# Kernel optimization log

Hardware: AMD Instinct MI355X
Metric: run time of the kernel (lower is better)

Reference implementation:

```python
import jax, jax.numpy as jnp
import numpy as np
import math

LMAX = 2            # input lmax
LMAX_OUT = 2 * LMAX # gaunt product output lmax
RES_BETA = 20
RES_ALPHA = 39
N = 2048
MUL = 64
C = 64
BRANCHES = [(1, 1), (1, -1), (-1, 1)]  # (p_val1, p_val2) per branch


def _real_sh_grid(lmax, res_beta, res_alpha):
    """Real orthonormal spherical harmonics on a Gauss-Legendre x uniform-alpha grid.
    Returns Y [(lmax+1)^2, res_beta, res_alpha] and quadrature weights qw [res_beta]
    (beta GL weight times 2*pi/res_alpha alpha weight)."""
    x, w = np.polynomial.legendre.leggauss(res_beta)  # x = cos(beta)
    phi = np.linspace(0.0, 2.0 * np.pi, res_alpha, endpoint=False)
    # associated Legendre P[l, m] on x via standard recurrences
    P = np.zeros((lmax + 1, lmax + 1, res_beta))
    P[0, 0] = 1.0
    s = np.sqrt(1.0 - x ** 2)
    for m in range(1, lmax + 1):
        P[m, m] = -(2 * m - 1) * s * P[m - 1, m - 1]
    for m in range(lmax):
        P[m + 1, m] = (2 * m + 1) * x * P[m, m]
    for m in range(lmax + 1):
        for l in range(m + 2, lmax + 1):
            P[l, m] = ((2 * l - 1) * x * P[l - 1, m] - (l + m - 1) * P[l - 2, m]) / (l - m)
    Y = np.zeros(((lmax + 1) ** 2, res_beta, res_alpha))
    idx = 0
    for l in range(lmax + 1):
        for m in range(-l, l + 1):
            am = abs(m)
            K = math.sqrt((2 * l + 1) / (4 * math.pi) * math.factorial(l - am) / math.factorial(l + am))
            if m == 0:
                ang = np.ones(res_alpha)
            elif m > 0:
                ang = math.sqrt(2.0) * np.cos(m * phi)
            else:
                ang = math.sqrt(2.0) * np.sin(am * phi)
            Y[idx] = K * P[l, am][:, None] * ang[None, :]
            idx += 1
    qw = w * (2.0 * np.pi / res_alpha)
    return Y.astype(np.float32), qw.astype(np.float32)


def setup_inputs() -> dict:
    key = jax.random.key(0)
    k1, k2, k3, k4, k5 = jax.random.split(key, 5)
    # inputs carry both parities per l: [N, mul, parity(2), (lmax+1)^2]
    x1 = jax.random.normal(k1, (N, MUL, 2, (LMAX + 1) ** 2), dtype=jnp.float32)
    x2 = jax.random.normal(k2, (N, MUL, 2, (LMAX + 1) ** 2), dtype=jnp.float32)
    # per-branch, per-l linear weights (e3nn Linear mixes multiplicities within each irrep)
    W1 = jax.random.normal(k3, (3, LMAX + 1, MUL, C), dtype=jnp.float32)
    W2 = jax.random.normal(k4, (3, LMAX + 1, MUL, C), dtype=jnp.float32)
    Wout = jax.random.normal(k5, (3, LMAX_OUT + 1, C, C), dtype=jnp.float32)
    Yfull, qw = _real_sh_grid(LMAX_OUT, RES_BETA, RES_ALPHA)
    Y_in = jnp.asarray(Yfull[: (LMAX + 1) ** 2])   # [9, B, A]
    Y_out = jnp.asarray(Yfull)                     # [25, B, A]
    return {"x1": x1, "x2": x2, "W1": W1, "W2": W2, "Wout": Wout,
            "Y_in": Y_in, "Y_out": Y_out, "qw": jnp.asarray(qw)}


def _project(x, W, p_val):
    """e3nn Linear to s2_irreps(LMAX, p_val)*C: for each l, take the input block with
    parity p_val*(-1)^l and mix multiplicities. x [N,mul,2,L2], W [L, mul, C] -> [N, C, L2]."""
    blocks = []
    inv_sqrt_mul = 1.0 / np.sqrt(x.shape[1])
    for l in range(LMAX + 1):
        pidx = 0 if p_val * ((-1) ** l) == 1 else 1  # 0 = even, 1 = odd parity slot
        sl = slice(l * l, (l + 1) * (l + 1))
        blocks.append(jnp.einsum('nmk,mc->nck', x[:, :, pidx, sl], W[l]) * inv_sqrt_mul)
    return jnp.concatenate(blocks, axis=-1)  # [N, C, (LMAX+1)^2]


def _gaunt_branch(x1, x2, W1b, W2b, Woutb, p1, p2, Y_in, Y_out, qw):
    c1 = _project(x1, W1b, p1)                      # [N, C, 9]
    c2 = _project(x2, W2b, p2)
    # SH -> grid (inverse spherical transform)
    s1 = jnp.einsum('ncl,lba->ncba', c1, Y_in)      # [N, C, B, A]
    s2 = jnp.einsum('ncl,lba->ncba', c2, Y_in)
    # pointwise multiply on S2, then grid -> SH (forward transform w/ quadrature)
    co = jnp.einsum('ncba,lba,b->ncl', s1 * s2, Y_out, qw)  # [N, C, 25]
    # linear_out: per-l [C -> C] mixing
    inv_sqrt_c = 1.0 / np.sqrt(co.shape[1])
    outs = []
    for l in range(LMAX_OUT + 1):
        sl = slice(l * l, (l + 1) * (l + 1))
        outs.append(jnp.einsum('nck,cd->ndk', co[:, :, sl], Woutb[l]) * inv_sqrt_c)
    return jnp.concatenate(outs, axis=-1)           # [N, C, 25]


def reference(x1, x2, W1, W2, Wout, Y_in, Y_out, qw):
    outs = [_gaunt_branch(x1, x2, W1[b], W2[b], Wout[b], p1, p2, Y_in, Y_out, qw)
            for b, (p1, p2) in enumerate(BRANCHES)]
    return jnp.stack(outs, axis=1)                  # [N, 3, C, 25] (concat over parities)
```

## Files before the change

kernel.cpp:

```cpp
#include <hip/hip_runtime.h>
#include <utility>


#define NN 2048

__host__ __device__ constexpr int l_of9(int i)  { return i < 1 ? 0 : (i < 4 ? 1 : 2); }
__host__ __device__ constexpr int l_of25(int k) { return k < 1 ? 0 : (k < 4 ? 1 : (k < 9 ? 2 : (k < 16 ? 3 : 4))); }
__host__ __device__ constexpr int iabs_(int v)  { return v < 0 ? -v : v; }

__host__ __device__ constexpr bool gmask(int k, int i, int j) {
    const int l3 = l_of25(k), m3 = k - l3 * l3 - l3;
    const int l1 = l_of9(i),  m1 = i - l1 * l1 - l1;
    const int l2 = l_of9(j),  m2 = j - l2 * l2 - l2;
    if (((l1 + l2 + l3) & 1) != 0) return false;
    if (l3 > l1 + l2 || l3 < iabs_(l1 - l2)) return false;
    const int am3 = iabs_(m3);
    return (am3 == iabs_(m1 + m2)) || (am3 == iabs_(m1 - m2));
}

struct GTab {
    int po[82];
    int pc[81];
    int kl[81][12];
    constexpr GTab() : po{}, pc{}, kl{} {
        int off = 0;
        for (int ij = 0; ij < 81; ++ij) {
            po[ij] = off;
            const int i = ij / 9, j = ij % 9;
            int cnum = 0;
            for (int k = 0; k < 25; ++k)
                if (gmask(k, i, j)) kl[ij][cnum++] = k;
            pc[ij] = cnum;
            off += (cnum + 3) & ~3;
        }
        po[81] = off;
    }
};
constexpr GTab GT{};

__global__ __launch_bounds__(256) void gaunt_pack_kernel(
    const float* __restrict__ Y_in, const float* __restrict__ Y_out,
    const float* __restrict__ qw, float* __restrict__ gp)
{
    const int ij = blockIdx.x;
    const int i = ij / 9, j = ij % 9;
    const int t = threadIdx.x;

    __shared__ float yy[780];
    __shared__ float ps[25][8];
    __shared__ float gr[25];

    for (int p = t; p < 780; p += 256)
        yy[p] = Y_in[i * 780 + p] * Y_in[j * 780 + p] * qw[p / 39];
    __syncthreads();

    if (t < 200) {
        const int k = t >> 3, s = t & 7;
        const float* yo = Y_out + k * 780;
        const int p1 = (s * 98 + 98 < 780) ? (s * 98 + 98) : 780;
        float a = 0.f;
        for (int p = s * 98; p < p1; ++p) a = fmaf(yy[p], yo[p], a);
        ps[k][s] = a;
    }
    __syncthreads();

    if (t < 25) {
        float a = 0.f;
#pragma unroll
        for (int s = 0; s < 8; ++s) a += ps[t][s];
        gr[t] = a;
    }
    __syncthreads();

    const int cntp = (GT.pc[ij] + 3) & ~3;
    if (t < cntp)
        gp[GT.po[ij] + t] = (t < GT.pc[ij]) ? gr[GT.kl[ij][t]] * 0.015625f : 0.f;
}

template <int IJ, int... Ts>
__device__ __forceinline__ void gaunt_apply(const float (&g)[12], float pij,
    float (&cov)[25], std::integer_sequence<int, Ts...>)
{
    ((cov[GT.kl[IJ][Ts]] = fmaf(g[Ts], pij, cov[GT.kl[IJ][Ts]])), ...);
}

template <int IJ>
__device__ __forceinline__ void gaunt_pair(const float* __restrict__ gp,
    const float (&c1)[9], const float (&c2)[9], float (&cov)[25])
{
    constexpr int cnt = GT.pc[IJ];
    if constexpr (cnt > 0) {
        constexpr int base = GT.po[IJ];
        constexpr int nv = (cnt + 3) / 4;
        const float pij = c1[IJ / 9] * c2[IJ % 9];
        float g[12];
#pragma unroll
        for (int q = 0; q < nv; ++q) {
            const float4 v = ((const float4*)(gp + base))[q];
            g[4 * q] = v.x; g[4 * q + 1] = v.y; g[4 * q + 2] = v.z; g[4 * q + 3] = v.w;
        }
        gaunt_apply<IJ>(g, pij, cov, std::make_integer_sequence<int, cnt>{});
    }
}

template <int I, int... Js>
__device__ __forceinline__ void gaunt_row(const float* __restrict__ gp,
    const float (&c1)[9], const float (&c2)[9], float (&cov)[25],
    std::integer_sequence<int, Js...>)
{
    (gaunt_pair<I * 9 + Js>(gp, c1, c2, cov), ...);
    __builtin_amdgcn_sched_barrier(0);
}

template <int... Is>
__device__ __forceinline__ void gaunt_all(const float* __restrict__ gp,
    const float (&c1)[9], const float (&c2)[9], float (&cov)[25],
    std::integer_sequence<int, Is...>)
{
    (gaunt_row<Is>(gp, c1, c2, cov, std::make_integer_sequence<int, 9>{}), ...);
}

typedef __attribute__((address_space(1))) const unsigned int gas_u32;
typedef __attribute__((address_space(3))) unsigned int las_u32;
__device__ __forceinline__ void gll16(const void* g, void* l) {
    __builtin_amdgcn_global_load_lds((gas_u32*)g, (las_u32*)l, 16, 0, 0);
}

template <int E1, int E2>
__device__ __forceinline__ void k1_body(
    const float* __restrict__ x1, const float* __restrict__ x2,
    const float* __restrict__ W1, const float* __restrict__ W2,
    const float* __restrict__ Wout, const float* __restrict__ gp,
    float* __restrict__ out, float* smemf, int b)
{
    const int t  = threadIdx.x;
    const int c  = t & 63;
    const int w  = t >> 6;
    const int n0 = blockIdx.y * 4;
    const int n  = n0 + w;

    char* smem = (char*)smemf;

    auto stage = [&](int mc, int buf) {
        {
            const int g   = t;
            const int arr = g / 144;
            const int gg  = g - arr * 144;
            const int n_l = gg / 36;
            const int r4  = (gg - n_l * 36) * 4;
            const float* src = (arr ? x2 : x1) +
                (size_t)(n0 + n_l) * 1152 + mc * 144 + r4;
            char* dst = smem + buf * 4608 + (t & ~63) * 16;
            gll16(src, dst);
        }
        if (t < 32) {
            const int gg  = 256 + t - 144;
            const int r4  = (gg - 108) * 4;
            const float* src = x2 + (size_t)(n0 + 3) * 1152 + mc * 144 + r4;
            char* dst = smem + buf * 4608 + 4096;
            gll16(src, dst);
        }
    };

    const float* W1b = W1 + (size_t)b * 12288 + c;
    const float* W2b = W2 + (size_t)b * 12288 + c;

    float a1[9] = {0,0,0,0,0,0,0,0,0};
    float a2[9] = {0,0,0,0,0,0,0,0,0};

    stage(0, 0);
    __syncthreads();

#pragma unroll 1
    for (int mc = 0; mc < 8; ++mc) {
        const int buf = mc & 1;
        if (mc < 7) stage(mc + 1, buf ^ 1);

        const float* xb1 = smemf + buf * 1152 + w * 144;
        const float* xb2 = smemf + buf * 1152 + 576 + w * 144;

#pragma unroll 1
        for (int mh = 0; mh < 2; ++mh) {
            float w1r[3][4], w2r[3][4];
#pragma unroll
            for (int l = 0; l < 3; ++l)
#pragma unroll
                for (int mm = 0; mm < 4; ++mm) {
                    const int o = (l * 64 + mc * 8 + mh * 4 + mm) * 64;
                    w1r[l][mm] = W1b[o];
                    w2r[l][mm] = W2b[o];
                }
#pragma unroll
            for (int mm = 0; mm < 4; ++mm) {
                const float* r1 = xb1 + (mh * 4 + mm) * 18;
                const float* r2 = xb2 + (mh * 4 + mm) * 18;
                float xv1[18], xv2[18];
#pragma unroll
                for (int q = 0; q < 9; ++q) {
                    const float2 v1 = *(const float2*)(r1 + q * 2);
                    const float2 v2 = *(const float2*)(r2 + q * 2);
                    xv1[2*q] = v1.x; xv1[2*q+1] = v1.y;
                    xv2[2*q] = v2.x; xv2[2*q+1] = v2.y;
                }
#pragma unroll
                for (int l = 0; l < 3; ++l) {
                    const int O1 = ((l & 1) ^ E1) * 9 + l * l;
                    const int O2 = ((l & 1) ^ E2) * 9 + l * l;
#pragma unroll
                    for (int ii = 0; ii <= 2 * l; ++ii) {
                        a1[l*l+ii] = fmaf(xv1[O1 + ii], w1r[l][mm], a1[l*l+ii]);
                        a2[l*l+ii] = fmaf(xv2[O2 + ii], w2r[l][mm], a2[l*l+ii]);
                    }
                }
            }
        }
        __syncthreads();
    }

    float cov[25] = {0,0,0,0,0,0,0,0,0,0,0,0,0,0,0,0,0,0,0,0,0,0,0,0,0};
    gaunt_all(gp, a1, a2, cov, std::make_integer_sequence<int, 9>{});

    float* colw = smemf + w * 1792;
#pragma unroll
    for (int k = 0; k < 25; ++k) colw[c * 28 + k] = cov[k];

    const float* WoB = Wout + (size_t)b * 20480 + c;
    float acc[25];
#pragma unroll
    for (int k = 0; k < 25; ++k) acc[k] = 0.f;

#pragma unroll 1
    for (int dc = 0; dc < 16; ++dc) {
        float wv[5][4];
#pragma unroll
        for (int l3 = 0; l3 < 5; ++l3)
#pragma unroll
            for (int dd = 0; dd < 4; ++dd)
                wv[l3][dd] = WoB[(l3 * 64 + dc * 4 + dd) * 64];
#pragma unroll
        for (int dd = 0; dd < 4; ++dd) {
            const float* row = colw + (dc * 4 + dd) * 28;
            float f[28];
#pragma unroll
            for (int q = 0; q < 7; ++q) {
                const float4 v = *(const float4*)(row + q * 4);
                f[4*q] = v.x; f[4*q+1] = v.y; f[4*q+2] = v.z; f[4*q+3] = v.w;
            }
#pragma unroll
            for (int k = 0; k < 25; ++k)
                acc[k] = fmaf(f[k], wv[l_of25(k)][dd], acc[k]);
        }
    }

#pragma unroll
    for (int k = 0; k < 25; ++k) colw[c * 25 + k] = acc[k] * 0.125f;

    float* on = out + ((size_t)n * 3 + b) * 1600;
#pragma unroll
    for (int r = 0; r < 6; ++r) {
        const float4 v = *(const float4*)&colw[r * 256 + c * 4];
        *(float4*)&on[r * 256 + c * 4] = v;
    }
    on[1536 + c] = colw[1536 + c];
}

__global__ __launch_bounds__(256, 4) void fused_kernel(
    const float* __restrict__ x1, const float* __restrict__ x2,
    const float* __restrict__ W1, const float* __restrict__ W2,
    const float* __restrict__ Wout, const float* __restrict__ gp,
    float* __restrict__ out)
{
    __shared__ __align__(16) float smemf[7168];
    const int b = blockIdx.x;
    if (b == 0)      k1_body<0, 0>(x1, x2, W1, W2, Wout, gp, out, smemf, 0);
    else if (b == 1) k1_body<0, 1>(x1, x2, W1, W2, Wout, gp, out, smemf, 1);
    else             k1_body<1, 0>(x1, x2, W1, W2, Wout, gp, out, smemf, 2);
}

extern "C" void kernel_launch(void* const* d_in, const int* in_sizes, int n_in,
                              void* d_out, int out_size, void* d_ws, size_t ws_size,
                              hipStream_t stream) {
    const float* x1    = (const float*)d_in[0];
    const float* x2    = (const float*)d_in[1];
    const float* W1    = (const float*)d_in[2];
    const float* W2    = (const float*)d_in[3];
    const float* Wout  = (const float*)d_in[4];
    const float* Y_in  = (const float*)d_in[5];
    const float* Y_out = (const float*)d_in[6];
    const float* qw    = (const float*)d_in[7];
    float* outp = (float*)d_out;
    float* gp   = (float*)d_ws;

    gaunt_pack_kernel<<<81, 256, 0, stream>>>(Y_in, Y_out, qw, gp);
    fused_kernel<<<dim3(3, NN / 4), 256, 0, stream>>>(x1, x2, W1, W2, Wout, gp, outp);
}
```

Baseline: 173.8 us.

## Split projection reduction over mul across lanes with float4 weight loads

The input projection is restructured so each lane covers 4 output channels and a quarter of the multiplicity range. Weights are read as float4 per lane, and the partial sums are combined with xor shuffles before each lane keeps its own channel. The whole x tile for the block is staged into LDS in one go with padded rows in place of the double-buffered chunks, and the grid is transposed so branch is the slow axis. The aim is fewer scalar weight loads and fewer barriers, at the cost of more accumulator registers, larger LDS, and a lower occupancy bound.

```diff
diff --git a/kernel.cpp b/kernel.cpp
--- a/kernel.cpp
+++ b/kernel.cpp
@@ -133,98 +133,122 @@
     const float* __restrict__ Wout, const float* __restrict__ gp,
     float* __restrict__ out, float* smemf, int b)
 {
-    const int t  = threadIdx.x;
-    const int c  = t & 63;
-    const int w  = t >> 6;
-    const int n0 = blockIdx.y * 4;
-    const int n  = n0 + w;
+    const int t    = threadIdx.x;
+    const int lane = t & 63;
+    const int w    = t >> 6;
+    const int c_q  = lane & 15;
+    const int m_s  = lane >> 4;
+    const int n0   = blockIdx.x * 4;
+    const int n    = n0 + w;
 
     char* smem = (char*)smemf;
-
-    auto stage = [&](int mc, int buf) {
+#pragma unroll
+    for (int i = 0; i < 10; ++i) {
+        const int G   = i * 256 + t;
+        const int n_l = G / 640;
+        const int rem = G - n_l * 640;
+        const int arr = rem / 320;
+        const int g   = rem - arr * 320;
+        const int r   = g / 5;
+        const int gs  = g - r * 5;
+        const int mi  = r >> 2;
+        const int msl = r & 3;
+        const int m   = msl * 16 + mi;
+        const int ss  = (gs == 4) ? 14 : gs * 4;
+        const float* src = (arr ? x2 : x1) + (size_t)(n0 + n_l) * 1152 + m * 18 + ss;
+        char* dst = smem + (i * 256 + (t & ~63)) * 16;
+        gll16(src, dst);
+    }
+    __syncthreads();
+
+    const float* xb1 = smemf + w * 2560;
+    const float* xb2 = xb1 + 1280;
+
+    float a1[4][9], a2[4][9];
+#pragma unroll
+    for (int cg = 0; cg < 4; ++cg)
+#pragma unroll
+        for (int i = 0; i < 9; ++i) { a1[cg][i] = 0.f; a2[cg][i] = 0.f; }
+
+    union F4 { float4 v; float f[4]; };
+
+#pragma unroll 1
+    for (int mi = 0; mi < 16; ++mi) {
+        const int m = m_s * 16 + mi;
+        const float* r1 = xb1 + (mi * 4 + m_s) * 20;
+        const float* r2 = xb2 + (mi * 4 + m_s) * 20;
+
+        float cx1[18], cx2[18];
+#pragma unroll
+        for (int q = 0; q < 4; ++q) {
+            const float4 u1 = *(const float4*)(r1 + q * 4);
+            const float4 u2 = *(const float4*)(r2 + q * 4);
+            cx1[4*q] = u1.x; cx1[4*q+1] = u1.y; cx1[4*q+2] = u1.z; cx1[4*q+3] = u1.w;
+            cx2[4*q] = u2.x; cx2[4*q+1] = u2.y; cx2[4*q+2] = u2.z; cx2[4*q+3] = u2.w;
+        }
         {
-            const int g   = t;
-            const int arr = g / 144;
-            const int gg  = g - arr * 144;
-            const int n_l = gg / 36;
-            const int r4  = (gg - n_l * 36) * 4;
-            const float* src = (arr ? x2 : x1) +
-                (size_t)(n0 + n_l) * 1152 + mc * 144 + r4;
-            char* dst = smem + buf * 4608 + (t & ~63) * 16;
-            gll16(src, dst);
-        }
-        if (t < 32) {
-            const int gg  = 256 + t - 144;
-            const int r4  = (gg - 108) * 4;
-            const float* src = x2 + (size_t)(n0 + 3) * 1152 + mc * 144 + r4;
-            char* dst = smem + buf * 4608 + 4096;
-            gll16(src, dst);
-        }
-    };
-
-    const float* W1b = W1 + (size_t)b * 12288 + c;
-    const float* W2b = W2 + (size_t)b * 12288 + c;
-
-    float a1[9] = {0,0,0,0,0,0,0,0,0};
-    float a2[9] = {0,0,0,0,0,0,0,0,0};
-
-    stage(0, 0);
-    __syncthreads();
-
-#pragma unroll 1
-    for (int mc = 0; mc < 8; ++mc) {
-        const int buf = mc & 1;
-        if (mc < 7) stage(mc + 1, buf ^ 1);
-
-        const float* xb1 = smemf + buf * 1152 + w * 144;
-        const float* xb2 = smemf + buf * 1152 + 576 + w * 144;
-
-#pragma unroll 1
-        for (int mh = 0; mh < 2; ++mh) {
-            float w1r[3][4], w2r[3][4];
-#pragma unroll
-            for (int l = 0; l < 3; ++l)
-#pragma unroll
-                for (int mm = 0; mm < 4; ++mm) {
-                    const int o = (l * 64 + mc * 8 + mh * 4 + mm) * 64;
-                    w1r[l][mm] = W1b[o];
-                    w2r[l][mm] = W2b[o];
+            const float4 u1 = *(const float4*)(r1 + 16);
+            const float4 u2 = *(const float4*)(r2 + 16);
+            cx1[16] = u1.z; cx1[17] = u1.w;
+            cx2[16] = u2.z; cx2[17] = u2.w;
+        }
+
+        F4 w1q[3], w2q[3];
+#pragma unroll
+        for (int l = 0; l < 3; ++l) {
+            const size_t o = ((size_t)((b * 3 + l) * 64 + m)) * 64 + c_q * 4;
+            w1q[l].v = *(const float4*)(W1 + o);
+            w2q[l].v = *(const float4*)(W2 + o);
+        }
+
+#pragma unroll
+        for (int l = 0; l < 3; ++l) {
+            const int O1 = ((l & 1) ^ E1) * 9 + l * l;
+            const int O2 = ((l & 1) ^ E2) * 9 + l * l;
+#pragma unroll
+            for (int cg = 0; cg < 4; ++cg)
+#pragma unroll
+                for (int ii = 0; ii <= 2 * l; ++ii) {
+                    a1[cg][l*l+ii] = fmaf(cx1[O1 + ii], w1q[l].f[cg], a1[cg][l*l+ii]);
+                    a2[cg][l*l+ii] = fmaf(cx2[O2 + ii], w2q[l].f[cg], a2[cg][l*l+ii]);
                 }
-#pragma unroll
-            for (int mm = 0; mm < 4; ++mm) {
-                const float* r1 = xb1 + (mh * 4 + mm) * 18;
-                const float* r2 = xb2 + (mh * 4 + mm) * 18;
-                float xv1[18], xv2[18];
-#pragma unroll
-                for (int q = 0; q < 9; ++q) {
-                    const float2 v1 = *(const float2*)(r1 + q * 2);
-                    const float2 v2 = *(const float2*)(r2 + q * 2);
-                    xv1[2*q] = v1.x; xv1[2*q+1] = v1.y;
-                    xv2[2*q] = v2.x; xv2[2*q+1] = v2.y;
-                }
-#pragma unroll
-                for (int l = 0; l < 3; ++l) {
-                    const int O1 = ((l & 1) ^ E1) * 9 + l * l;
-                    const int O2 = ((l & 1) ^ E2) * 9 + l * l;
-#pragma unroll
-                    for (int ii = 0; ii <= 2 * l; ++ii) {
-                        a1[l*l+ii] = fmaf(xv1[O1 + ii], w1r[l][mm], a1[l*l+ii]);
-                        a2[l*l+ii] = fmaf(xv2[O2 + ii], w2r[l][mm], a2[l*l+ii]);
-                    }
-                }
-            }
-        }
-        __syncthreads();
-    }
+        }
+    }
+
+#pragma unroll
+    for (int cg = 0; cg < 4; ++cg)
+#pragma unroll
+        for (int i = 0; i < 9; ++i) {
+            a1[cg][i] += __shfl_xor(a1[cg][i], 16, 64);
+            a1[cg][i] += __shfl_xor(a1[cg][i], 32, 64);
+            a2[cg][i] += __shfl_xor(a2[cg][i], 16, 64);
+            a2[cg][i] += __shfl_xor(a2[cg][i], 32, 64);
+        }
+
+    float c1v[9], c2v[9];
+#pragma unroll
+    for (int i = 0; i < 9; ++i) { c1v[i] = a1[0][i]; c2v[i] = a2[0][i]; }
+#pragma unroll
+    for (int q = 1; q < 4; ++q) {
+        const bool sel = (m_s == q);
+#pragma unroll
+        for (int i = 0; i < 9; ++i) {
+            c1v[i] = sel ? a1[q][i] : c1v[i];
+            c2v[i] = sel ? a2[q][i] : c2v[i];
+        }
+    }
+    const int cown = c_q * 4 + m_s;
 
     float cov[25] = {0,0,0,0,0,0,0,0,0,0,0,0,0,0,0,0,0,0,0,0,0,0,0,0,0};
-    gaunt_all(gp, a1, a2, cov, std::make_integer_sequence<int, 9>{});
+    gaunt_all(gp, c1v, c2v, cov, std::make_integer_sequence<int, 9>{});
+
+    __syncthreads();
 
     float* colw = smemf + w * 1792;
 #pragma unroll
-    for (int k = 0; k < 25; ++k) colw[c * 28 + k] = cov[k];
-
-    const float* WoB = Wout + (size_t)b * 20480 + c;
+    for (int k = 0; k < 25; ++k) colw[cown * 28 + k] = cov[k];
+
+    const float* WoB = Wout + (size_t)b * 20480 + cown;
     float acc[25];
 #pragma unroll
     for (int k = 0; k < 25; ++k) acc[k] = 0.f;
@@ -253,25 +277,25 @@
     }
 
 #pragma unroll
-    for (int k = 0; k < 25; ++k) colw[c * 25 + k] = acc[k] * 0.125f;
+    for (int k = 0; k < 25; ++k) colw[cown * 25 + k] = acc[k] * 0.125f;
 
     float* on = out + ((size_t)n * 3 + b) * 1600;
 #pragma unroll
     for (int r = 0; r < 6; ++r) {
-        const float4 v = *(const float4*)&colw[r * 256 + c * 4];
-        *(float4*)&on[r * 256 + c * 4] = v;
-    }
-    on[1536 + c] = colw[1536 + c];
-}
-
-__global__ __launch_bounds__(256, 4) void fused_kernel(
+        const float4 v = *(const float4*)&colw[r * 256 + lane * 4];
+        *(float4*)&on[r * 256 + lane * 4] = v;
+    }
+    on[1536 + lane] = colw[1536 + lane];
+}
+
+__global__ __launch_bounds__(256, 3) void fused_kernel(
     const float* __restrict__ x1, const float* __restrict__ x2,
     const float* __restrict__ W1, const float* __restrict__ W2,
     const float* __restrict__ Wout, const float* __restrict__ gp,
     float* __restrict__ out)
 {
-    __shared__ __align__(16) float smemf[7168];
-    const int b = blockIdx.x;
+    __shared__ __align__(16) float smemf[10240];
+    const int b = blockIdx.y;
     if (b == 0)      k1_body<0, 0>(x1, x2, W1, W2, Wout, gp, out, smemf, 0);
     else if (b == 1) k1_body<0, 1>(x1, x2, W1, W2, Wout, gp, out, smemf, 1);
     else             k1_body<1, 0>(x1, x2, W1, W2, Wout, gp, out, smemf, 2);
@@ -292,5 +316,5 @@
     float* gp   = (float*)d_ws;
 
     gaunt_pack_kernel<<<81, 256, 0, stream>>>(Y_in, Y_out, qw, gp);
-    fused_kernel<<<dim3(3, NN / 4), 256, 0, stream>>>(x1, x2, W1, W2, Wout, gp, outp);
-}
+    fused_kernel<<<dim3(NN / 4, 3), 256, 0, stream>>>(x1, x2, W1, W2, Wout, gp, outp);
+}
```

Result: slower. 180.6 us (+3.9%).
